# Kernel tuning notes

Measured on AMD Instinct MI355X. Metric: run time of the kernel, lower is better.

The kernel has to match this reference:

```python
import jax, jax.numpy as jnp
import numpy as np

N_NODES = 50000   # gates in the circuit batch
N_HOPS = 100000   # number of k-hop cones
MAX_PI = 8        # max PIs per hop (padded, masked via stats == -1)
D = 128           # token_emb / hidden
D_FF = 4 * D      # cls_head hidden width (512)
TT = 64           # max_tt_len -> logits width
LN_EPS = 1e-5


def setup_inputs() -> dict:
    key = jax.random.key(0)
    ks = jax.random.split(key, 8)
    hf = jax.random.normal(ks[0], (N_NODES, D), jnp.float32)
    all_hop_pi = jax.random.randint(ks[1], (N_HOPS, MAX_PI), 0, N_NODES)
    # stats in {-1, 0, 1}; -1 marks an invalid (padded) PI slot
    all_hop_pi_stats = jax.random.randint(ks[2], (N_HOPS, MAX_PI), 0, 3) - 1
    all_hop_po = jax.random.randint(ks[3], (N_HOPS,), 0, N_NODES)
    w_q = jax.random.normal(ks[4], (D,), jnp.float32) / np.sqrt(D)
    W1 = jax.random.normal(ks[5], (D, D_FF), jnp.float32) / np.sqrt(D)
    b1 = jnp.zeros((D_FF,), jnp.float32)
    gamma = jnp.ones((D_FF,), jnp.float32)
    beta = jnp.zeros((D_FF,), jnp.float32)
    W2 = jax.random.normal(ks[6], (D_FF, TT), jnp.float32) / np.sqrt(D_FF)
    b2 = jnp.zeros((TT,), jnp.float32)
    return {
        'hf': hf, 'w_q': w_q, 'W1': W1, 'b1': b1, 'gamma': gamma,
        'beta': beta, 'W2': W2, 'b2': b2,
        'all_hop_pi': all_hop_pi, 'all_hop_pi_stats': all_hop_pi_stats,
        'all_hop_po': all_hop_po,
    }


def reference(hf, w_q, W1, b1, gamma, beta, W2, b2,
              all_hop_pi, all_hop_pi_stats, all_hop_po):
    # Per-hop gather: valid PI embeddings + PO embedding -> [H, P+1, D]
    pi_tok = hf[all_hop_pi]                       # [H, P, D]
    po_tok = hf[all_hop_po][:, None, :]           # [H, 1, D]
    tokens = jnp.concatenate([pi_tok, po_tok], axis=1)
    valid = jnp.concatenate(
        [all_hop_pi_stats != -1,
         jnp.ones((all_hop_po.shape[0], 1), bool)], axis=1)  # [H, P+1]
    # tf_Pooling: masked single-query attention pooling over the ragged set
    scores = jnp.einsum('hpd,d->hp', tokens, w_q) / jnp.sqrt(jnp.float32(D))
    scores = jnp.where(valid, scores, jnp.float32(-1e30))
    attn = jax.nn.softmax(scores, axis=-1)
    hop_hf = jnp.einsum('hp,hpd->hd', attn, tokens)  # [H, D]
    # cls_head: Linear(D, 4D) -> ReLU -> LayerNorm(4D) -> Linear(4D, TT)
    h = jax.nn.relu(hop_hf @ W1 + b1)
    mu = jnp.mean(h, axis=-1, keepdims=True)
    var = jnp.var(h, axis=-1, keepdims=True)
    h = (h - mu) * jax.lax.rsqrt(var + LN_EPS) * gamma + beta
    logits = h @ W2 + b2                           # [H, TT]
    return logits
```

## Files before the change

kernel.cpp:

```cpp
#include <hip/hip_runtime.h>
#include <hip/hip_bf16.h>
#include <math.h>

#define DIM 128
#define DFF 512
#define TTW 64
#define NPI 8
#define NTOK 9
#define TILE_H 32

typedef __attribute__((ext_vector_type(8))) short short8;
typedef __attribute__((ext_vector_type(4))) float float4v;

__device__ __forceinline__ float bf16lo_f32(unsigned u) {
    union { unsigned u; float f; } v; v.u = u << 16;
    return v.f;
}
__device__ __forceinline__ float bf16hi_f32(unsigned u) {
    union { unsigned u; float f; } v; v.u = u & 0xffff0000u;
    return v.f;
}
__device__ __forceinline__ unsigned pk_bf16(float a, float b) {
    __hip_bfloat162 h = __float22bfloat162_rn(float2{a, b});
    union { __hip_bfloat162 h; unsigned u; } cv; cv.h = h;
    return cv.u;
}

__global__ __launch_bounds__(256)
void prep_k(const float* __restrict__ hf, const float* __restrict__ W1,
            const float* __restrict__ W2, const int* __restrict__ pi,
            const int* __restrict__ stats,
            unsigned short* __restrict__ hf2, unsigned short* __restrict__ w1t,
            unsigned short* __restrict__ w2t, int* __restrict__ cpack,
            int n_hf, int B_HF, int n_pk)
{
    __shared__ float tile[32][33];
    const int b = blockIdx.x, t = threadIdx.x;
    if (b < B_HF) {
        int i = (b * 256 + t) * 4;
        if (i < n_hf) {
            float4v v = *(const float4v*)(hf + i);
            uint2 o;
            o.x = pk_bf16(v[0], v[1]);
            o.y = pk_bf16(v[2], v[3]);
            *(uint2*)(hf2 + i) = o;
        }
    } else if (b < B_HF + 64) {
        const int tb = b - B_HF;
        const int r0 = (tb & 3) * 32, c0 = (tb >> 2) * 32;
        const int ty = t >> 3, tx = t & 7;
        *(float4v*)&tile[ty][tx * 4] = *(const float4v*)(W1 + (r0 + ty) * DFF + c0 + tx * 4);
        __syncthreads();
        uint2 o;
        o.x = pk_bf16(tile[tx * 4 + 0][ty], tile[tx * 4 + 1][ty]);
        o.y = pk_bf16(tile[tx * 4 + 2][ty], tile[tx * 4 + 3][ty]);
        *(uint2*)(w1t + (c0 + ty) * DIM + r0 + tx * 4) = o;
    } else if (b < B_HF + 96) {
        const int tb = b - B_HF - 64;
        const int r0 = (tb & 15) * 32, c0 = (tb >> 4) * 32;
        const int ty = t >> 3, tx = t & 7;
        *(float4v*)&tile[ty][tx * 4] = *(const float4v*)(W2 + (r0 + ty) * TTW + c0 + tx * 4);
        __syncthreads();
        uint2 o;
        o.x = pk_bf16(tile[tx * 4 + 0][ty], tile[tx * 4 + 1][ty]);
        o.y = pk_bf16(tile[tx * 4 + 2][ty], tile[tx * 4 + 3][ty]);
        *(uint2*)(w2t + (c0 + ty) * DFF + r0 + tx * 4) = o;
    } else {
        const int pb = b - (B_HF + 96);
        int i = (pb * 256 + t) * 4;
        if (i < n_pk) {
            int4 p = *(const int4*)(pi + i);
            int4 s = *(const int4*)(stats + i);
            int4 o;
            o.x = p.x | (s.x == -1 ? (int)0x80000000 : 0);
            o.y = p.y | (s.y == -1 ? (int)0x80000000 : 0);
            o.z = p.z | (s.z == -1 ? (int)0x80000000 : 0);
            o.w = p.w | (s.w == -1 ? (int)0x80000000 : 0);
            *(int4*)(cpack + i) = o;
        }
    }
}

__global__ __launch_bounds__(256, 3)
void fused_k(const unsigned short* __restrict__ hf2,
             const float* __restrict__ w_q,
             const int* __restrict__ cpack,
             const int* __restrict__ po,
             const unsigned short* __restrict__ w1t,
             const float* __restrict__ b1,
             const float* __restrict__ gamma,
             const float* __restrict__ beta,
             const unsigned short* __restrict__ w2t,
             const float* __restrict__ b2,
             float* __restrict__ out,
             int H)
{
    __shared__ unsigned short Apool[TILE_H][DIM + 8];
    __shared__ unsigned short Hsm[TILE_H][DFF + 8];
    __shared__ float part[2][16][4][2];

    const int t    = threadIdx.x;
    const int lane = t & 63;
    const int w    = t >> 6;
    const int row  = lane & 15;
    const int quad = lane >> 4;
    const int hop0 = blockIdx.x * TILE_H;

    {
        const int g = t >> 5, l = t & 31;
        const float4v wq4 = *(const float4v*)(w_q + l * 4);
        #pragma unroll
        for (int it = 0; it < 4; ++it) {
            const int hl = g + it * 8;
            const int hop = hop0 + hl;
            uint2 o = {0u, 0u};
            if (hop < H) {
                int idx[NTOK]; bool val[NTOK];
                int4 c0 = *(const int4*)(cpack + hop * NPI);
                int4 c1 = *(const int4*)(cpack + hop * NPI + 4);
                idx[0]=c0.x & 0x7fffffff; val[0]=c0.x >= 0;
                idx[1]=c0.y & 0x7fffffff; val[1]=c0.y >= 0;
                idx[2]=c0.z & 0x7fffffff; val[2]=c0.z >= 0;
                idx[3]=c0.w & 0x7fffffff; val[3]=c0.w >= 0;
                idx[4]=c1.x & 0x7fffffff; val[4]=c1.x >= 0;
                idx[5]=c1.y & 0x7fffffff; val[5]=c1.y >= 0;
                idx[6]=c1.z & 0x7fffffff; val[6]=c1.z >= 0;
                idx[7]=c1.w & 0x7fffffff; val[7]=c1.w >= 0;
                idx[8]=po[hop]; val[8]=true;
                uint2 tu[NTOK];
                #pragma unroll
                for (int p = 0; p < NTOK; ++p)
                    tu[p] = *(const uint2*)(hf2 + (size_t)idx[p] * DIM + l * 4);
                float tok[NTOK][4];
                #pragma unroll
                for (int p = 0; p < NTOK; ++p) {
                    tok[p][0] = bf16lo_f32(tu[p].x);
                    tok[p][1] = bf16hi_f32(tu[p].x);
                    tok[p][2] = bf16lo_f32(tu[p].y);
                    tok[p][3] = bf16hi_f32(tu[p].y);
                }
                float sc[NTOK];
                #pragma unroll
                for (int p = 0; p < NTOK; ++p)
                    sc[p] = tok[p][0]*wq4[0] + tok[p][1]*wq4[1]
                          + tok[p][2]*wq4[2] + tok[p][3]*wq4[3];
                #pragma unroll
                for (int m = 1; m < 32; m <<= 1) {
                    #pragma unroll
                    for (int p = 0; p < NTOK; ++p) sc[p] += __shfl_xor(sc[p], m);
                }
                const float isd = 0.08838834764831845f;
                float mx = -1e30f;
                #pragma unroll
                for (int p = 0; p < NTOK; ++p) {
                    sc[p] = val[p] ? sc[p] * isd : -1e30f;
                    mx = fmaxf(mx, sc[p]);
                }
                float se = 0.f;
                #pragma unroll
                for (int p = 0; p < NTOK; ++p) { sc[p] = __expf(sc[p] - mx); se += sc[p]; }
                const float inv = 1.f / se;
                float a0=0.f, a1=0.f, a2=0.f, a3=0.f;
                #pragma unroll
                for (int p = 0; p < NTOK; ++p) {
                    float a = sc[p] * inv;
                    a0 += a * tok[p][0]; a1 += a * tok[p][1];
                    a2 += a * tok[p][2]; a3 += a * tok[p][3];
                }
                o.x = pk_bf16(a0, a1);
                o.y = pk_bf16(a2, a3);
            }
            *(uint2*)&Apool[hl][l * 4] = o;
        }
    }
    __syncthreads();

    float4v acc[8][2];
    #pragma unroll
    for (int mt = 0; mt < 8; ++mt) {
        acc[mt][0] = (float4v){0.f, 0.f, 0.f, 0.f};
        acc[mt][1] = (float4v){0.f, 0.f, 0.f, 0.f};
    }
    {
        short8 bfr[2][4];
        #pragma unroll
        for (int ks = 0; ks < 4; ++ks) {
            const int k0 = ks * 32 + quad * 8;
            #pragma unroll
            for (int ht = 0; ht < 2; ++ht)
                bfr[ht][ks] = *(const short8*)&Apool[ht * 16 + row][k0];
        }
        #pragma unroll
        for (int mt = 0; mt < 8; ++mt) {
            const unsigned short* wrow = w1t + (size_t)(w * 128 + mt * 16 + row) * DIM;
            #pragma unroll
            for (int ks = 0; ks < 4; ++ks) {
                short8 afr = *(const short8*)(wrow + ks * 32 + quad * 8);
                acc[mt][0] = __builtin_amdgcn_mfma_f32_16x16x32_bf16(afr, bfr[0][ks], acc[mt][0], 0, 0, 0);
                acc[mt][1] = __builtin_amdgcn_mfma_f32_16x16x32_bf16(afr, bfr[1][ks], acc[mt][1], 0, 0, 0);
            }
        }
    }
    float sum0 = 0.f, ssq0 = 0.f, sum1 = 0.f, ssq1 = 0.f;
    #pragma unroll
    for (int mt = 0; mt < 8; ++mt) {
        const int nb = w * 128 + mt * 16 + quad * 4;
        const float4v bias = *(const float4v*)(b1 + nb);
        #pragma unroll
        for (int r = 0; r < 4; ++r) {
            float v0 = fmaxf(acc[mt][0][r] + bias[r], 0.f);
            float v1 = fmaxf(acc[mt][1][r] + bias[r], 0.f);
            acc[mt][0][r] = v0;  sum0 += v0;  ssq0 += v0 * v0;
            acc[mt][1][r] = v1;  sum1 += v1;  ssq1 += v1 * v1;
        }
    }
    #pragma unroll
    for (int m = 16; m <= 32; m <<= 1) {
        sum0 += __shfl_xor(sum0, m);  ssq0 += __shfl_xor(ssq0, m);
        sum1 += __shfl_xor(sum1, m);  ssq1 += __shfl_xor(ssq1, m);
    }
    if (lane < 16) {
        part[0][row][w][0] = sum0;  part[0][row][w][1] = ssq0;
        part[1][row][w][0] = sum1;  part[1][row][w][1] = ssq1;
    }
    __syncthreads();
    float mu[2], rs[2];
    #pragma unroll
    for (int ht = 0; ht < 2; ++ht) {
        float S = 0.f, Q = 0.f;
        #pragma unroll
        for (int ww = 0; ww < 4; ++ww) {
            S += part[ht][row][ww][0];
            Q += part[ht][row][ww][1];
        }
        const float invn = 1.f / (float)DFF;
        mu[ht] = S * invn;
        float var = Q * invn - mu[ht] * mu[ht];
        rs[ht] = rsqrtf(var + 1e-5f);
    }
    #pragma unroll
    for (int mt = 0; mt < 8; ++mt) {
        const int nb = w * 128 + mt * 16 + quad * 4;
        const float4v g4  = *(const float4v*)(gamma + nb);
        const float4v be4 = *(const float4v*)(beta + nb);
        #pragma unroll
        for (int ht = 0; ht < 2; ++ht) {
            float o[4];
            #pragma unroll
            for (int r = 0; r < 4; ++r) {
                float tg = rs[ht] * g4[r];
                o[r] = acc[mt][ht][r] * tg + (be4[r] - mu[ht] * tg);
            }
            uint2 p;
            p.x = pk_bf16(o[0], o[1]);
            p.y = pk_bf16(o[2], o[3]);
            *(uint2*)&Hsm[ht * 16 + row][nb] = p;
        }
    }
    __syncthreads();

    {
        float4v acc2[2];
        acc2[0] = (float4v){0.f,0.f,0.f,0.f};
        acc2[1] = (float4v){0.f,0.f,0.f,0.f};
        #pragma unroll
        for (int ks = 0; ks < 16; ++ks) {
            const int k0 = ks * 32 + quad * 8;
            short8 bfr = *(const short8*)(w2t + (size_t)(w * 16 + row) * DFF + k0);
            #pragma unroll
            for (int mt = 0; mt < 2; ++mt) {
                short8 afr = *(const short8*)&Hsm[mt * 16 + row][k0];
                acc2[mt] = __builtin_amdgcn_mfma_f32_16x16x32_bf16(
                    afr, bfr, acc2[mt], 0, 0, 0);
            }
        }
        const float bb = b2[w * 16 + row];
        #pragma unroll
        for (int mt = 0; mt < 2; ++mt) {
            #pragma unroll
            for (int r = 0; r < 4; ++r) {
                int hop = hop0 + mt * 16 + quad * 4 + r;
                if (hop < H)
                    out[(size_t)hop * TTW + w * 16 + row] = acc2[mt][r] + bb;
            }
        }
    }
}

extern "C" void kernel_launch(void* const* d_in, const int* in_sizes, int n_in,
                              void* d_out, int out_size, void* d_ws, size_t ws_size,
                              hipStream_t stream) {
    const float* hf    = (const float*)d_in[0];
    const float* w_q   = (const float*)d_in[1];
    const float* W1    = (const float*)d_in[2];
    const float* b1    = (const float*)d_in[3];
    const float* gamma = (const float*)d_in[4];
    const float* beta  = (const float*)d_in[5];
    const float* W2    = (const float*)d_in[6];
    const float* b2    = (const float*)d_in[7];
    const int* pi      = (const int*)d_in[8];
    const int* stats   = (const int*)d_in[9];
    const int* po      = (const int*)d_in[10];
    float* out         = (float*)d_out;

    const int n_hf = in_sizes[0];
    const int H    = in_sizes[10];
    const int n_pk = H * NPI;

    char* ws = (char*)d_ws;
    unsigned short* w1t    = (unsigned short*)ws;
    unsigned short* w2t    = (unsigned short*)(ws + 131072);
    unsigned short* hf2    = (unsigned short*)(ws + 196608);
    size_t off_cp = 196608 + ((size_t)n_hf * 2 + 255) / 256 * 256;
    int*            cpack  = (int*)(ws + off_cp);

    const int B_HF = (n_hf + 1023) / 1024;
    const int B_PK = (n_pk + 1023) / 1024;
    const int prep_blocks = B_HF + 96 + B_PK;

    hipLaunchKernelGGL(prep_k, dim3(prep_blocks), dim3(256), 0, stream,
                       hf, W1, W2, pi, stats, hf2, w1t, w2t, cpack,
                       n_hf, B_HF, n_pk);
    hipLaunchKernelGGL(fused_k, dim3((H + TILE_H - 1) / TILE_H), dim3(256), 0, stream,
                       hf2, w_q, cpack, po, w1t, b1, gamma, beta, w2t, b2, out, H);
}
```

Baseline: 212.4 us.

## Drop index packing pass, alias pooled tile into hidden LDS, raise occupancy

Removes the prep pass that packed PI indices and validity into one int array; the fused kernel now reads pi and stats directly, trading one write plus re-read for a second 32-byte load per hop. The pooled-activation tile now aliases the start of the hidden-layer LDS buffer, which cuts shared memory and lets launch bounds ask for 4 blocks per CU instead of 3. The bf16 conversion of hf now handles 8 elements per thread with 16-byte stores. Aliasing relies on Apool being fully consumed before Hsm is written, and the higher occupancy target may force register spills.

```diff
diff --git a/kernel.cpp b/kernel.cpp
--- a/kernel.cpp
+++ b/kernel.cpp
@@ -28,22 +28,24 @@
 
 __global__ __launch_bounds__(256)
 void prep_k(const float* __restrict__ hf, const float* __restrict__ W1,
-            const float* __restrict__ W2, const int* __restrict__ pi,
-            const int* __restrict__ stats,
+            const float* __restrict__ W2,
             unsigned short* __restrict__ hf2, unsigned short* __restrict__ w1t,
-            unsigned short* __restrict__ w2t, int* __restrict__ cpack,
-            int n_hf, int B_HF, int n_pk)
+            unsigned short* __restrict__ w2t,
+            int n_hf, int B_HF)
 {
     __shared__ float tile[32][33];
     const int b = blockIdx.x, t = threadIdx.x;
     if (b < B_HF) {
-        int i = (b * 256 + t) * 4;
+        int i = (b * 256 + t) * 8;
         if (i < n_hf) {
-            float4v v = *(const float4v*)(hf + i);
-            uint2 o;
-            o.x = pk_bf16(v[0], v[1]);
-            o.y = pk_bf16(v[2], v[3]);
-            *(uint2*)(hf2 + i) = o;
+            float4v v0 = *(const float4v*)(hf + i);
+            float4v v1 = *(const float4v*)(hf + i + 4);
+            uint4 o;
+            o.x = pk_bf16(v0[0], v0[1]);
+            o.y = pk_bf16(v0[2], v0[3]);
+            o.z = pk_bf16(v1[0], v1[1]);
+            o.w = pk_bf16(v1[2], v1[3]);
+            *(uint4*)(hf2 + i) = o;
         }
     } else if (b < B_HF + 64) {
         const int tb = b - B_HF;
@@ -55,7 +57,7 @@
         o.x = pk_bf16(tile[tx * 4 + 0][ty], tile[tx * 4 + 1][ty]);
         o.y = pk_bf16(tile[tx * 4 + 2][ty], tile[tx * 4 + 3][ty]);
         *(uint2*)(w1t + (c0 + ty) * DIM + r0 + tx * 4) = o;
-    } else if (b < B_HF + 96) {
+    } else {
         const int tb = b - B_HF - 64;
         const int r0 = (tb & 15) * 32, c0 = (tb >> 4) * 32;
         const int ty = t >> 3, tx = t & 7;
@@ -65,26 +67,14 @@
         o.x = pk_bf16(tile[tx * 4 + 0][ty], tile[tx * 4 + 1][ty]);
         o.y = pk_bf16(tile[tx * 4 + 2][ty], tile[tx * 4 + 3][ty]);
         *(uint2*)(w2t + (c0 + ty) * DFF + r0 + tx * 4) = o;
-    } else {
-        const int pb = b - (B_HF + 96);
-        int i = (pb * 256 + t) * 4;
-        if (i < n_pk) {
-            int4 p = *(const int4*)(pi + i);
-            int4 s = *(const int4*)(stats + i);
-            int4 o;
-            o.x = p.x | (s.x == -1 ? (int)0x80000000 : 0);
-            o.y = p.y | (s.y == -1 ? (int)0x80000000 : 0);
-            o.z = p.z | (s.z == -1 ? (int)0x80000000 : 0);
-            o.w = p.w | (s.w == -1 ? (int)0x80000000 : 0);
-            *(int4*)(cpack + i) = o;
-        }
-    }
-}
-
-__global__ __launch_bounds__(256, 3)
+    }
+}
+
+__global__ __launch_bounds__(256, 4)
 void fused_k(const unsigned short* __restrict__ hf2,
              const float* __restrict__ w_q,
-             const int* __restrict__ cpack,
+             const int* __restrict__ pi,
+             const int* __restrict__ stats,
              const int* __restrict__ po,
              const unsigned short* __restrict__ w1t,
              const float* __restrict__ b1,
@@ -95,9 +85,9 @@
              float* __restrict__ out,
              int H)
 {
-    __shared__ unsigned short Apool[TILE_H][DIM + 8];
-    __shared__ unsigned short Hsm[TILE_H][DFF + 8];
+    __shared__ __align__(16) unsigned short Hsm[TILE_H][DFF + 8];
     __shared__ float part[2][16][4][2];
+    unsigned short (*Apool)[DIM + 8] = (unsigned short (*)[DIM + 8])&Hsm[0][0];
 
     const int t    = threadIdx.x;
     const int lane = t & 63;
@@ -116,16 +106,18 @@
             uint2 o = {0u, 0u};
             if (hop < H) {
                 int idx[NTOK]; bool val[NTOK];
-                int4 c0 = *(const int4*)(cpack + hop * NPI);
-                int4 c1 = *(const int4*)(cpack + hop * NPI + 4);
-                idx[0]=c0.x & 0x7fffffff; val[0]=c0.x >= 0;
-                idx[1]=c0.y & 0x7fffffff; val[1]=c0.y >= 0;
-                idx[2]=c0.z & 0x7fffffff; val[2]=c0.z >= 0;
-                idx[3]=c0.w & 0x7fffffff; val[3]=c0.w >= 0;
-                idx[4]=c1.x & 0x7fffffff; val[4]=c1.x >= 0;
-                idx[5]=c1.y & 0x7fffffff; val[5]=c1.y >= 0;
-                idx[6]=c1.z & 0x7fffffff; val[6]=c1.z >= 0;
-                idx[7]=c1.w & 0x7fffffff; val[7]=c1.w >= 0;
+                int4 p0 = *(const int4*)(pi + hop * NPI);
+                int4 p1 = *(const int4*)(pi + hop * NPI + 4);
+                int4 s0 = *(const int4*)(stats + hop * NPI);
+                int4 s1 = *(const int4*)(stats + hop * NPI + 4);
+                idx[0]=p0.x; val[0]=s0.x != -1;
+                idx[1]=p0.y; val[1]=s0.y != -1;
+                idx[2]=p0.z; val[2]=s0.z != -1;
+                idx[3]=p0.w; val[3]=s0.w != -1;
+                idx[4]=p1.x; val[4]=s1.x != -1;
+                idx[5]=p1.y; val[5]=s1.y != -1;
+                idx[6]=p1.z; val[6]=s1.z != -1;
+                idx[7]=p1.w; val[7]=s1.w != -1;
                 idx[8]=po[hop]; val[8]=true;
                 uint2 tu[NTOK];
                 #pragma unroll
@@ -305,22 +297,17 @@
 
     const int n_hf = in_sizes[0];
     const int H    = in_sizes[10];
-    const int n_pk = H * NPI;
 
     char* ws = (char*)d_ws;
-    unsigned short* w1t    = (unsigned short*)ws;
-    unsigned short* w2t    = (unsigned short*)(ws + 131072);
-    unsigned short* hf2    = (unsigned short*)(ws + 196608);
-    size_t off_cp = 196608 + ((size_t)n_hf * 2 + 255) / 256 * 256;
-    int*            cpack  = (int*)(ws + off_cp);
-
-    const int B_HF = (n_hf + 1023) / 1024;
-    const int B_PK = (n_pk + 1023) / 1024;
-    const int prep_blocks = B_HF + 96 + B_PK;
+    unsigned short* w1t = (unsigned short*)ws;
+    unsigned short* w2t = (unsigned short*)(ws + 131072);
+    unsigned short* hf2 = (unsigned short*)(ws + 196608);
+
+    const int B_HF = (n_hf + 2047) / 2048;
+    const int prep_blocks = B_HF + 96;
 
     hipLaunchKernelGGL(prep_k, dim3(prep_blocks), dim3(256), 0, stream,
-                       hf, W1, W2, pi, stats, hf2, w1t, w2t, cpack,
-                       n_hf, B_HF, n_pk);
+                       hf, W1, W2, hf2, w1t, w2t, n_hf, B_HF);
     hipLaunchKernelGGL(fused_k, dim3((H + TILE_H - 1) / TILE_H), dim3(256), 0, stream,
-                       hf2, w_q, cpack, po, w1t, b1, gamma, beta, w2t, b2, out, H);
-}
+                       hf2, w_q, pi, stats, po, w1t, b1, gamma, beta, w2t, b2, out, H);
+}
```

Result: slower. 251.7 us (+18.5%).
